# Kernel tuning notes

Measured on AMD Instinct MI355X. Metric: run time of the kernel, lower is better.

## Reference

```python
import jax, jax.numpy as jnp
import numpy as np


def _mlp(x, w1, b1, w2, b2):
    # Linear->ReLU->Linear->ReLU (torch Linear: y = x @ W.T + b)
    return jax.nn.relu(jax.nn.relu(x @ w1.T + b1) @ w2.T + b2)


def _lstm_cell(x, h, c, wih, whh, bih, bhh):
    g = x @ wih.T + bih + h @ whh.T + bhh
    i, f, gg, o = jnp.split(g, 4, axis=-1)  # torch gate order i,f,g,o
    c = jax.nn.sigmoid(f) * c + jax.nn.sigmoid(i) * jnp.tanh(gg)
    h = jax.nn.sigmoid(o) * jnp.tanh(c)
    return h, c


def _decode(iml, img_features, mlp1_w1, mlp1_b1, mlp1_w2, mlp1_b2,
            mlp2_w1, mlp2_b1, mlp2_w2, mlp2_b2,
            lstm_wih, lstm_whh, lstm_bih, lstm_bhh,
            attn_w, attn_b, fc_w, fc_b, emb, max_seq_len):
    # iml: [B, H, K] flattened conv map; annotations are channel vectors per position
    ann = jnp.transpose(iml, (0, 2, 1))          # [B, K, H]
    mean_ann = jnp.mean(iml, axis=-1)            # [B, H]
    h0 = _mlp(mean_ann, mlp1_w1, mlp1_b1, mlp1_w2, mlp1_b2)
    c0 = _mlp(mean_ann, mlp2_w1, mlp2_b1, mlp2_w2, mlp2_b2)
    H = h0.shape[-1]
    # attn = Linear(2H, 1) on cat(ann, h): decompose into two dot products.
    w_a, w_h = attn_w[:H], attn_w[H:]
    e_ann = ann @ w_a + attn_b[0]                # [B, K], annotation part precomputed

    def step(carry, _):
        x, h, c = carry
        h, c = _lstm_cell(x, h, c, lstm_wih, lstm_whh, lstm_bih, lstm_bhh)
        e = e_ann + (h @ w_h)[:, None]           # [B, K] fused concat+linear scores
        alpha = jax.nn.softmax(e, axis=-1)       # [B, K]
        cs = jnp.einsum('bk,bkh->bh', alpha, ann)  # weighted context [B, H]
        logits = jnp.concatenate([h, cs], axis=-1) @ fc_w.T + fc_b  # [B, V]
        sample = jnp.argmax(logits, axis=-1)     # greedy token
        return (emb[sample], h, c), (logits, sample)

    _, (logits, samples) = jax.lax.scan(step, (img_features, h0, c0), None, length=max_seq_len)
    # scan stacks on axis 0 (time); move to [B, T, ...]
    return jnp.transpose(logits, (1, 0, 2)), jnp.transpose(samples, (1, 0))


def setup_inputs() -> dict:
    B, K, H, E, V, T = 64, 196, 512, 512, 10000, 30
    key = jax.random.key(0)
    ks = jax.random.split(key, 11)
    inv = 1.0 / np.sqrt(H)
    r = lambda i, shape, scale=1.0: jax.random.normal(ks[i], shape, jnp.float32) * scale
    return {
        'iml': r(0, (B, H, K)),
        'img_features': r(1, (B, E)),
        'mlp1_w1': r(2, (H, H), inv), 'mlp1_b1': jnp.zeros(H, jnp.float32),
        'mlp1_w2': r(3, (H, H), inv), 'mlp1_b2': jnp.zeros(H, jnp.float32),
        'mlp2_w1': r(4, (H, H), inv), 'mlp2_b1': jnp.zeros(H, jnp.float32),
        'mlp2_w2': r(5, (H, H), inv), 'mlp2_b2': jnp.zeros(H, jnp.float32),
        'lstm_wih': r(6, (4 * H, E), inv), 'lstm_whh': r(7, (4 * H, H), inv),
        'lstm_bih': jnp.zeros(4 * H, jnp.float32), 'lstm_bhh': jnp.zeros(4 * H, jnp.float32),
        'attn_w': r(8, (2 * H,), inv), 'attn_b': jnp.zeros(1, jnp.float32),
        'fc_w': r(9, (V, 2 * H), inv), 'fc_b': jnp.zeros(V, jnp.float32),
        'emb': r(10, (V, E)),
        'max_seq_len': T,
    }


def reference(iml, img_features, mlp1_w1, mlp1_b1, mlp1_w2, mlp1_b2,
              mlp2_w1, mlp2_b1, mlp2_w2, mlp2_b2,
              lstm_wih, lstm_whh, lstm_bih, lstm_bhh,
              attn_w, attn_b, fc_w, fc_b, emb, max_seq_len):
    all_logits, sampled_ids = _decode(
        iml, img_features, mlp1_w1, mlp1_b1, mlp1_w2, mlp1_b2,
        mlp2_w1, mlp2_b1, mlp2_w2, mlp2_b2,
        lstm_wih, lstm_whh, lstm_bih, lstm_bhh,
        attn_w, attn_b, fc_w, fc_b, emb, max_seq_len)
    return all_logits, sampled_ids
```

## Files before the change

kernel.cpp:

```cpp
#include <hip/hip_runtime.h>
#include <hip/hip_bf16.h>

#define B 64
#define KDIM 196
#define H 512
#define V 10000
#define TSTEPS 30
#define VP 10240
#define NVC 40
#define NSLOT 8
#define SLOTSTRIDE 16
#define NT 256

typedef unsigned long long u64;
typedef unsigned int u32;

__device__ __forceinline__ u64 pack_vi(float v, int idx) {
    u32 kb = __float_as_uint(v);
    kb = (kb & 0x80000000u) ? ~kb : (kb | 0x80000000u);
    return ((u64)kb << 32) | (u32)(~(u32)idx);
}
__device__ __forceinline__ u32 best_idx_of_slots(const u64* __restrict__ slots, int b) {
    u64 best = slots[b * SLOTSTRIDE];
#pragma unroll
    for (int s = 1; s < NSLOT; ++s) { u64 v = slots[b * SLOTSTRIDE + s]; if (v > best) best = v; }
    return ~(u32)best;
}


__global__ void k_transpose_fc(const float* __restrict__ fcw, float* __restrict__ dst, int coloff) {
    __shared__ float tile[32][33];
    int v0 = blockIdx.x * 32, i0 = blockIdx.y * 32;
    int tx = threadIdx.x, ty = threadIdx.y;
#pragma unroll
    for (int r = 0; r < 32; r += 8) {
        int v = v0 + ty + r; int i = i0 + tx;
        tile[ty + r][tx] = (v < V) ? fcw[(size_t)v * 1024 + coloff + i] : 0.f;
    }
    __syncthreads();
#pragma unroll
    for (int r = 0; r < 32; r += 8) {
        int i = i0 + ty + r; int v = v0 + tx;
        dst[(size_t)i * VP + v] = tile[tx][ty + r];
    }
}

__global__ void k_build_wct(const float* __restrict__ wih, const float* __restrict__ whh,
                            float* __restrict__ dst) {
    __shared__ float tile[32][33];
    int j0 = blockIdx.x * 32, i0 = blockIdx.y * 32;
    int tx = threadIdx.x, ty = threadIdx.y;
#pragma unroll
    for (int r = 0; r < 32; r += 8) {
        int j = j0 + ty + r; int i = i0 + tx;
        tile[ty + r][tx] = (i < 512) ? wih[(size_t)j * 512 + i] : whh[(size_t)j * 512 + i - 512];
    }
    __syncthreads();
#pragma unroll
    for (int r = 0; r < 32; r += 8) {
        int i = i0 + ty + r; int j = j0 + tx;
        dst[(size_t)i * 2048 + j] = tile[tx][ty + r];
    }
}

__global__ void k_e_alpha(const float* __restrict__ iml, const float* __restrict__ attn_w,
                          float* __restrict__ alpha) {
    int b = blockIdx.x, t = threadIdx.x;
    __shared__ float wa[512];
    wa[t] = attn_w[t]; wa[t + 256] = attn_w[t + 256];
    __syncthreads();
    float acc = 0.f;
    if (t < KDIM) {
        const float* p = iml + (size_t)b * 512 * KDIM + t;
#pragma unroll 8
        for (int h = 0; h < 512; ++h) acc += p[(size_t)h * KDIM] * wa[h];
    }
    __shared__ float red[256];
    red[t] = (t < KDIM) ? acc : -__builtin_inff();
    __syncthreads();
    for (int s = 128; s; s >>= 1) { if (t < s) red[t] = fmaxf(red[t], red[t + s]); __syncthreads(); }
    float mx = red[0];
    __syncthreads();
    float ex = (t < KDIM) ? expf(acc - mx) : 0.f;
    red[t] = ex; __syncthreads();
    for (int s = 128; s; s >>= 1) { if (t < s) red[t] += red[t + s]; __syncthreads(); }
    if (t < KDIM) alpha[b * KDIM + t] = ex / red[0];
}

__global__ void k_mean_cs(const float* __restrict__ iml, const float* __restrict__ alpha,
                          float* __restrict__ mean, float* __restrict__ cs) {
    int w = threadIdx.x >> 6, lane = threadIdx.x & 63;
    int row = blockIdx.x * 4 + w;
    int b = row >> 9;
    const float* p = iml + (size_t)row * KDIM;
    const float* al = alpha + b * KDIM;
    float p0 = p[lane], p1 = p[lane + 64], p2 = p[lane + 128];
    float p3 = (lane < 4) ? p[lane + 192] : 0.f;
    float a3 = (lane < 4) ? al[lane + 192] : 0.f;
    float sm = p0 + p1 + p2 + p3;
    float sc = p0 * al[lane] + p1 * al[lane + 64] + p2 * al[lane + 128] + p3 * a3;
#pragma unroll
    for (int off = 32; off; off >>= 1) { sm += __shfl_down(sm, off); sc += __shfl_down(sc, off); }
    if (lane == 0) { mean[row] = sm * (1.f / 196.f); cs[row] = sc; }
}

__global__ void k_dense_relu2(const float* __restrict__ in0, const float* __restrict__ in1,
                              const float* __restrict__ W0, const float* __restrict__ W1,
                              const float* __restrict__ bi0, const float* __restrict__ bi1,
                              float* __restrict__ o0, float* __restrict__ o1) {
    int z = blockIdx.z;
    const float* in = z ? in1 : in0;
    const float* W  = z ? W1 : W0;
    const float* bias = z ? bi1 : bi0;
    float* out = z ? o1 : o0;
    int b = blockIdx.y; int j = blockIdx.x * 256 + threadIdx.x;
    __shared__ float xs[512];
    xs[threadIdx.x] = in[b * 512 + threadIdx.x];
    xs[threadIdx.x + 256] = in[b * 512 + threadIdx.x + 256];
    __syncthreads();
    float acc = bias[j];
    const float4* w4 = (const float4*)(W + (size_t)j * 512);
#pragma unroll 4
    for (int i4 = 0; i4 < 128; ++i4) {
        float4 w = w4[i4];
        float4 x = *(const float4*)&xs[i4 * 4];
        acc += w.x * x.x + w.y * x.y + w.z * x.z + w.w * x.w;
    }
    out[(size_t)b * 512 + j] = fmaxf(acc, 0.f);
}

__global__ void k_gemm_big(const float* __restrict__ A, int astride,
                           const float* __restrict__ Wt, int wn,
                           float* __restrict__ part) {
    int jb = blockIdx.x, kc = blockIdx.y, bh = blockIdx.z;
    int w = threadIdx.x >> 6, lane = threadIdx.x & 63;
    int b0 = __builtin_amdgcn_readfirstlane(bh * 32 + w * 8);
    int k0 = kc * 64;
    int j0 = jb * 256 + lane * 4;
    float4 acc[8];
#pragma unroll
    for (int b = 0; b < 8; ++b) acc[b] = make_float4(0.f, 0.f, 0.f, 0.f);
    const float* wp = Wt + (size_t)k0 * wn + j0;
    const float* xp = A + (size_t)b0 * astride + k0;
#pragma unroll 8
    for (int kk = 0; kk < 64; ++kk) {
        float4 w4 = *(const float4*)(wp + (size_t)kk * wn);
#pragma unroll
        for (int b = 0; b < 8; ++b) {
            float xv = xp[(size_t)b * astride + kk];
            acc[b].x += xv * w4.x; acc[b].y += xv * w4.y;
            acc[b].z += xv * w4.z; acc[b].w += xv * w4.w;
        }
    }
#pragma unroll
    for (int b = 0; b < 8; ++b)
        *(float4*)(part + (size_t)(kc * 64 + b0 + b) * wn + j0) = acc[b];
}

__global__ void k_base_finish(const float* __restrict__ lpart, const float* __restrict__ fc_b,
                              float* __restrict__ base, u64* __restrict__ slots) {
    int b = blockIdx.y; int v = blockIdx.x * 256 + threadIdx.x;
    if (v < V) {
        float s = fc_b[v];
#pragma unroll
        for (int c = 0; c < 8; ++c) s += lpart[(size_t)(c * 64 + b) * VP + v];
        base[(size_t)b * VP + v] = s;
    }
    if (blockIdx.x == 0 && blockIdx.y == 0) {
#pragma unroll
        for (int i = 0; i < 4; ++i) slots[threadIdx.x + i * 256] = 0ull;
    }
}


__global__ __launch_bounds__(NT) void k_lstm(
        const float* __restrict__ img, const float* __restrict__ emb,
        const u64* __restrict__ slots, const float* __restrict__ hbuf,
        const float* __restrict__ WcT, float* __restrict__ gpart, int t0) {
    __shared__ float lds[4 * 1024];
    const int jb = blockIdx.x, kc = blockIdx.y, bh = blockIdx.z;
    const int tid = threadIdx.x;
    const int w = __builtin_amdgcn_readfirstlane(tid >> 6), lane = tid & 63;
    const int b0 = bh * 8;
    const int kg0 = kc * 256 + w * 64;
    const float* xp[8];
    if (kg0 < 512) {
        if (t0) {
#pragma unroll
            for (int b = 0; b < 8; ++b) xp[b] = img + (size_t)(b0 + b) * 512 + kg0;
        } else {
#pragma unroll
            for (int b = 0; b < 8; ++b) {
                u32 idx = best_idx_of_slots(slots, b0 + b);
                xp[b] = emb + (size_t)idx * 512 + kg0;
            }
        }
    } else {
#pragma unroll
        for (int b = 0; b < 8; ++b) xp[b] = hbuf + (size_t)(b0 + b) * 512 + (kg0 - 512);
    }
    float2 acc[8];
#pragma unroll
    for (int b = 0; b < 8; ++b) acc[b] = make_float2(0.f, 0.f);
    const float* wp = WcT + (size_t)kg0 * 2048 + jb * 128 + lane * 2;
#pragma unroll 8
    for (int kk = 0; kk < 64; ++kk) {
        float2 wv = *(const float2*)(wp + (size_t)kk * 2048);
#pragma unroll
        for (int b = 0; b < 8; ++b) {
            float xv = xp[b][kk];
            acc[b].x += xv * wv.x; acc[b].y += xv * wv.y;
        }
    }
#pragma unroll
    for (int b = 0; b < 8; ++b)
        *(float2*)&lds[w * 1024 + b * 128 + lane * 2] = acc[b];
    __syncthreads();
    {
        const int bl = tid >> 5;
        const int jj = (tid & 31) * 4;
        float4 s = make_float4(0.f, 0.f, 0.f, 0.f);
#pragma unroll
        for (int wv = 0; wv < 4; ++wv) {
            float4 p = *(const float4*)&lds[wv * 1024 + bl * 128 + jj];
            s.x += p.x; s.y += p.y; s.z += p.z; s.w += p.w;
        }
        *(float4*)&gpart[(size_t)(kc * 64 + b0 + bl) * 2048 + jb * 128 + jj] = s;
    }
}

__global__ void k_gates(const float* __restrict__ gpart, const float* __restrict__ bih,
                        const float* __restrict__ bhh, float* __restrict__ hbuf,
                        float* __restrict__ cbuf, u64* __restrict__ slots,
                        float* __restrict__ out1, int t) {
    int e = blockIdx.x * 256 + threadIdx.x;
    int b = e >> 9, jj = e & 511;
    float g[4];
#pragma unroll
    for (int gg = 0; gg < 4; ++gg) {
        int j = jj + gg * 512;
        float s = bih[j] + bhh[j];
#pragma unroll
        for (int kc = 0; kc < 4; ++kc) s += gpart[(size_t)(kc * 64 + b) * 2048 + j];
        g[gg] = s;
    }
    float ig = 1.f / (1.f + expf(-g[0]));
    float fg = 1.f / (1.f + expf(-g[1]));
    float gt = tanhf(g[2]);
    float og = 1.f / (1.f + expf(-g[3]));
    float c = fg * cbuf[e] + ig * gt;
    float h = og * tanhf(c);
    cbuf[e] = c; hbuf[e] = h;
    if (blockIdx.x == 0) {
        if (t > 0 && threadIdx.x < 64)
            out1[threadIdx.x * TSTEPS + (t - 1)] = (float)best_idx_of_slots(slots, threadIdx.x);
        __syncthreads();
        for (int i = threadIdx.x; i < B * SLOTSTRIDE; i += 256) slots[i] = 0ull;
    }
}

__global__ __launch_bounds__(NT) void k_logits_fullk(
        const float* __restrict__ hbuf, const float* __restrict__ fcT,
        const float* __restrict__ base, float* __restrict__ out0,
        u64* __restrict__ slots, int t) {
    __shared__ float lds[4 * 1280];
    const int jb = blockIdx.x, bh = blockIdx.y;
    const int tid = threadIdx.x;
    const int w = __builtin_amdgcn_readfirstlane(tid >> 6), lane = tid & 63;
    const int b0 = bh * 8;
    const int kg0 = w * 128;
    float2 a2[8]; float a1[8];
#pragma unroll
    for (int b = 0; b < 8; ++b) { a2[b] = make_float2(0.f, 0.f); a1[b] = 0.f; }
    const float* wp2 = fcT + (size_t)kg0 * VP + jb * 160 + lane * 2;
    const float* wp1 = fcT + (size_t)kg0 * VP + jb * 160 + 128 + (lane & 31);
    const float* hb0 = hbuf + (size_t)b0 * 512 + kg0;
#pragma unroll 4
    for (int kk = 0; kk < 128; ++kk) {
        float2 w2 = *(const float2*)(wp2 + (size_t)kk * VP);
        float w1 = wp1[(size_t)kk * VP];
#pragma unroll
        for (int b = 0; b < 8; ++b) {
            float xv = hb0[b * 512 + kk];
            a2[b].x += xv * w2.x; a2[b].y += xv * w2.y; a1[b] += xv * w1;
        }
    }
#pragma unroll
    for (int b = 0; b < 8; ++b)
        *(float2*)&lds[w * 1280 + b * 160 + lane * 2] = a2[b];
    if (lane < 32) {
#pragma unroll
        for (int b = 0; b < 8; ++b) lds[w * 1280 + b * 160 + 128 + lane] = a1[b];
    }
    __syncthreads();
    {
        const int bl = tid >> 5;
        const int jj0 = (tid & 31) * 5;
        const int bg = b0 + bl;
        const int j0 = jb * 160 + jj0;
        float m = -__builtin_inff(); int mi = 0x7fffffff;
        if (j0 < V) {
            float* op = out0 + ((size_t)bg * TSTEPS + t) * V + j0;
            const float* bp = base + (size_t)bg * VP + j0;
#pragma unroll
            for (int i = 0; i < 5; ++i) {
                float s = 0.f;
#pragma unroll
                for (int wv = 0; wv < 4; ++wv) s += lds[wv * 1280 + bl * 160 + jj0 + i];
                float val = s + bp[i];
                op[i] = val;
                if (val > m) { m = val; mi = j0 + i; }
            }
        }
#pragma unroll
        for (int mk = 1; mk < 32; mk <<= 1) {
            float ov = __shfl_xor(m, mk);
            int oi = __shfl_xor(mi, mk);
            if (ov > m || (ov == m && oi < mi)) { m = ov; mi = oi; }
        }
        if ((lane & 31) == 0)
            atomicMax(&slots[bg * SLOTSTRIDE + (jb & 7)], pack_vi(m, mi));
    }
}

__global__ void k_final_out1(const u64* __restrict__ slots, float* __restrict__ out1) {
    int b = threadIdx.x;
    if (b < B) out1[b * TSTEPS + (TSTEPS - 1)] = (float)best_idx_of_slots(slots, b);
}


extern "C" void kernel_launch(void* const* d_in, const int* in_sizes, int n_in,
                              void* d_out, int out_size, void* d_ws, size_t ws_size,
                              hipStream_t stream) {
    const float* iml   = (const float*)d_in[0];
    const float* img   = (const float*)d_in[1];
    const float* m1w1  = (const float*)d_in[2];
    const float* m1b1  = (const float*)d_in[3];
    const float* m1w2  = (const float*)d_in[4];
    const float* m1b2  = (const float*)d_in[5];
    const float* m2w1  = (const float*)d_in[6];
    const float* m2b1  = (const float*)d_in[7];
    const float* m2w2  = (const float*)d_in[8];
    const float* m2b2  = (const float*)d_in[9];
    const float* wih   = (const float*)d_in[10];
    const float* whh   = (const float*)d_in[11];
    const float* bih   = (const float*)d_in[12];
    const float* bhh   = (const float*)d_in[13];
    const float* attnw = (const float*)d_in[14];
    const float* fcw   = (const float*)d_in[16];
    const float* fcb   = (const float*)d_in[17];
    const float* emb   = (const float*)d_in[18];

    float* out0 = (float*)d_out;
    float* out1 = out0 + (size_t)B * TSTEPS * V;

    float* ws = (float*)d_ws;
    size_t off = 0;
    float* fcT   = ws + off; off += (size_t)512 * VP;
    float* WcT   = ws + off; off += (size_t)1024 * 2048;
    float* bigp  = ws + off; off += (size_t)8 * B * VP;
    float* gpart = ws + off; off += (size_t)4 * B * 2048;
    float* base  = ws + off; off += (size_t)B * VP;
    float* meanb = ws + off; off += B * 512;
    float* alpha = ws + off; off += B * KDIM;
    float* csb   = ws + off; off += B * 512;
    float* tmp1  = ws + off; off += B * 512;
    float* tmp2  = ws + off; off += B * 512;
    float* hbuf  = ws + off; off += B * 512;
    float* cbuf  = ws + off; off += B * 512;
    u64*   slots = (u64*)(ws + off); off += B * SLOTSTRIDE * 2;

    k_e_alpha<<<dim3(64), dim3(256), 0, stream>>>(iml, attnw, alpha);
    k_mean_cs<<<dim3(8192), dim3(256), 0, stream>>>(iml, alpha, meanb, csb);
    k_dense_relu2<<<dim3(2, 64, 2), dim3(256), 0, stream>>>(meanb, meanb, m1w1, m2w1, m1b1, m2b1, tmp1, tmp2);
    k_dense_relu2<<<dim3(2, 64, 2), dim3(256), 0, stream>>>(tmp1, tmp2, m1w2, m2w2, m1b2, m2b2, hbuf, cbuf);
    k_transpose_fc<<<dim3(VP / 32, 16), dim3(32, 8), 0, stream>>>(fcw, fcT, 512);
    k_gemm_big<<<dim3(40, 8, 2), dim3(256), 0, stream>>>(csb, 512, fcT, VP, bigp);
    k_base_finish<<<dim3(NVC, 64), dim3(256), 0, stream>>>(bigp, fcb, base, slots);
    k_transpose_fc<<<dim3(VP / 32, 16), dim3(32, 8), 0, stream>>>(fcw, fcT, 0);
    k_build_wct<<<dim3(64, 32), dim3(32, 8), 0, stream>>>(wih, whh, WcT);

    for (int t = 0; t < TSTEPS; ++t) {
        k_lstm<<<dim3(16, 4, 8), dim3(NT), 0, stream>>>(img, emb, slots, hbuf, WcT, gpart, (t == 0) ? 1 : 0);
        k_gates<<<dim3(128), dim3(256), 0, stream>>>(gpart, bih, bhh, hbuf, cbuf, slots, out1, t);
        k_logits_fullk<<<dim3(64, 8), dim3(NT), 0, stream>>>(hbuf, fcT, base, out0, slots, t);
    }
    k_final_out1<<<dim3(1), dim3(64), 0, stream>>>(slots, out1);
}
```

Measured before the change: 1.342 ms.

## Fuse LSTM gate activation into logits kernel with double-buffered state

Removes the separate per-step gates kernel. Each logits block now rebuilds the h vectors for its 8 batch rows from the gate partial sums and keeps them in shared memory. The cell state and the argmax slots are double-buffered, so the redundant per-block gate work causes no races, and the slot reset and output write move into the LSTM kernel. The attention score reduction is also split across more blocks, and the bias sum is precomputed. The cost is that every one of the 64 column blocks recomputes the gates, which repeats gpart reads and transcendental math, traded against one fewer launch and sync per step.

```diff
diff --git a/kernel.cpp b/kernel.cpp
--- a/kernel.cpp
+++ b/kernel.cpp
@@ -10,6 +10,7 @@
 #define NVC 40
 #define NSLOT 8
 #define SLOTSTRIDE 16
+#define SLOTBUF (B * SLOTSTRIDE)
 #define NT 256
 
 typedef unsigned long long u64;
@@ -63,17 +64,33 @@
     }
 }
 
-__global__ void k_e_alpha(const float* __restrict__ iml, const float* __restrict__ attn_w,
-                          float* __restrict__ alpha) {
+__global__ void k_bsum(const float* __restrict__ bih, const float* __restrict__ bhh,
+                       float* __restrict__ bsum) {
+    int j = blockIdx.x * 256 + threadIdx.x;
+    bsum[j] = bih[j] + bhh[j];
+}
+
+__global__ void k_e_part(const float* __restrict__ iml, const float* __restrict__ attn_w,
+                         float* __restrict__ epart) {
+    int b = blockIdx.x, hc = blockIdx.y, t = threadIdx.x;
+    __shared__ float wa[64];
+    if (t < 64) wa[t] = attn_w[hc * 64 + t];
+    __syncthreads();
+    if (t < KDIM) {
+        const float* p = iml + (size_t)b * 512 * KDIM + (size_t)hc * 64 * KDIM + t;
+        float acc = 0.f;
+#pragma unroll 8
+        for (int h = 0; h < 64; ++h) acc += p[(size_t)h * KDIM] * wa[h];
+        epart[(size_t)(b * 8 + hc) * 208 + t] = acc;
+    }
+}
+
+__global__ void k_e_softmax(const float* __restrict__ epart, float* __restrict__ alpha) {
     int b = blockIdx.x, t = threadIdx.x;
-    __shared__ float wa[512];
-    wa[t] = attn_w[t]; wa[t + 256] = attn_w[t + 256];
-    __syncthreads();
     float acc = 0.f;
     if (t < KDIM) {
-        const float* p = iml + (size_t)b * 512 * KDIM + t;
-#pragma unroll 8
-        for (int h = 0; h < 512; ++h) acc += p[(size_t)h * KDIM] * wa[h];
+#pragma unroll
+        for (int c = 0; c < 8; ++c) acc += epart[(size_t)(b * 8 + c) * 208 + t];
     }
     __shared__ float red[256];
     red[t] = (t < KDIM) ? acc : -__builtin_inff();
@@ -175,8 +192,9 @@
 
 __global__ __launch_bounds__(NT) void k_lstm(
         const float* __restrict__ img, const float* __restrict__ emb,
-        const u64* __restrict__ slots, const float* __restrict__ hbuf,
-        const float* __restrict__ WcT, float* __restrict__ gpart, int t0) {
+        const u64* __restrict__ slotsR, u64* __restrict__ slotsW,
+        const float* __restrict__ hbuf, const float* __restrict__ WcT,
+        float* __restrict__ gpart, float* __restrict__ out1, int t) {
     __shared__ float lds[4 * 1024];
     const int jb = blockIdx.x, kc = blockIdx.y, bh = blockIdx.z;
     const int tid = threadIdx.x;
@@ -185,13 +203,13 @@
     const int kg0 = kc * 256 + w * 64;
     const float* xp[8];
     if (kg0 < 512) {
-        if (t0) {
+        if (t == 0) {
 #pragma unroll
             for (int b = 0; b < 8; ++b) xp[b] = img + (size_t)(b0 + b) * 512 + kg0;
         } else {
 #pragma unroll
             for (int b = 0; b < 8; ++b) {
-                u32 idx = best_idx_of_slots(slots, b0 + b);
+                u32 idx = best_idx_of_slots(slotsR, b0 + b);
                 xp[b] = emb + (size_t)idx * 512 + kg0;
             }
         }
@@ -227,61 +245,65 @@
         }
         *(float4*)&gpart[(size_t)(kc * 64 + b0 + bl) * 2048 + jb * 128 + jj] = s;
     }
-}
-
-__global__ void k_gates(const float* __restrict__ gpart, const float* __restrict__ bih,
-                        const float* __restrict__ bhh, float* __restrict__ hbuf,
-                        float* __restrict__ cbuf, u64* __restrict__ slots,
-                        float* __restrict__ out1, int t) {
-    int e = blockIdx.x * 256 + threadIdx.x;
-    int b = e >> 9, jj = e & 511;
-    float g[4];
-#pragma unroll
-    for (int gg = 0; gg < 4; ++gg) {
-        int j = jj + gg * 512;
-        float s = bih[j] + bhh[j];
-#pragma unroll
-        for (int kc = 0; kc < 4; ++kc) s += gpart[(size_t)(kc * 64 + b) * 2048 + j];
-        g[gg] = s;
-    }
-    float ig = 1.f / (1.f + expf(-g[0]));
-    float fg = 1.f / (1.f + expf(-g[1]));
-    float gt = tanhf(g[2]);
-    float og = 1.f / (1.f + expf(-g[3]));
-    float c = fg * cbuf[e] + ig * gt;
-    float h = og * tanhf(c);
-    cbuf[e] = c; hbuf[e] = h;
-    if (blockIdx.x == 0) {
-        if (t > 0 && threadIdx.x < 64)
-            out1[threadIdx.x * TSTEPS + (t - 1)] = (float)best_idx_of_slots(slots, threadIdx.x);
-        __syncthreads();
-        for (int i = threadIdx.x; i < B * SLOTSTRIDE; i += 256) slots[i] = 0ull;
-    }
-}
-
-__global__ __launch_bounds__(NT) void k_logits_fullk(
-        const float* __restrict__ hbuf, const float* __restrict__ fcT,
+    if (jb == 0 && kc == 0 && t > 0 && tid < 8)
+        out1[(b0 + tid) * TSTEPS + (t - 1)] = (float)best_idx_of_slots(slotsR, b0 + tid);
+    if (jb == 1 && kc == 0 && bh == 0) {
+#pragma unroll
+        for (int i = 0; i < 4; ++i) slotsW[tid + i * 256] = 0ull;
+    }
+}
+
+__global__ __launch_bounds__(NT) void k_fused(
+        const float* __restrict__ gpart, const float* __restrict__ bsum,
+        const float* __restrict__ cbufR, float* __restrict__ cbufW,
+        float* __restrict__ hbuf, const float* __restrict__ fcT,
         const float* __restrict__ base, float* __restrict__ out0,
-        u64* __restrict__ slots, int t) {
+        u64* __restrict__ slotsW, int t) {
+    __shared__ float hs[8 * 512];
     __shared__ float lds[4 * 1280];
     const int jb = blockIdx.x, bh = blockIdx.y;
     const int tid = threadIdx.x;
+    const int b0 = bh * 8;
+#pragma unroll 4
+    for (int e = tid; e < 4096; e += NT) {
+        int b = e >> 9, jj = e & 511;
+        float g[4];
+#pragma unroll
+        for (int gg = 0; gg < 4; ++gg) {
+            int j = jj + gg * 512;
+            float s = bsum[j];
+#pragma unroll
+            for (int kc = 0; kc < 4; ++kc) s += gpart[(size_t)(kc * 64 + b0 + b) * 2048 + j];
+            g[gg] = s;
+        }
+        float ig = 1.f / (1.f + expf(-g[0]));
+        float fg = 1.f / (1.f + expf(-g[1]));
+        float gt = tanhf(g[2]);
+        float og = 1.f / (1.f + expf(-g[3]));
+        float c = fg * cbufR[(size_t)(b0 + b) * 512 + jj] + ig * gt;
+        float h = og * tanhf(c);
+        hs[b * 512 + jj] = h;
+        if (jb == 0) {
+            cbufW[(size_t)(b0 + b) * 512 + jj] = c;
+            hbuf[(size_t)(b0 + b) * 512 + jj] = h;
+        }
+    }
+    __syncthreads();
     const int w = __builtin_amdgcn_readfirstlane(tid >> 6), lane = tid & 63;
-    const int b0 = bh * 8;
     const int kg0 = w * 128;
     float2 a2[8]; float a1[8];
 #pragma unroll
     for (int b = 0; b < 8; ++b) { a2[b] = make_float2(0.f, 0.f); a1[b] = 0.f; }
     const float* wp2 = fcT + (size_t)kg0 * VP + jb * 160 + lane * 2;
     const float* wp1 = fcT + (size_t)kg0 * VP + jb * 160 + 128 + (lane & 31);
-    const float* hb0 = hbuf + (size_t)b0 * 512 + kg0;
+    const float* hsw = &hs[kg0];
 #pragma unroll 4
     for (int kk = 0; kk < 128; ++kk) {
         float2 w2 = *(const float2*)(wp2 + (size_t)kk * VP);
         float w1 = wp1[(size_t)kk * VP];
 #pragma unroll
         for (int b = 0; b < 8; ++b) {
-            float xv = hb0[b * 512 + kk];
+            float xv = hsw[b * 512 + kk];
             a2[b].x += xv * w2.x; a2[b].y += xv * w2.y; a1[b] += xv * w1;
         }
     }
@@ -318,8 +340,8 @@
             int oi = __shfl_xor(mi, mk);
             if (ov > m || (ov == m && oi < mi)) { m = ov; mi = oi; }
         }
-        if ((lane & 31) == 0)
-            atomicMax(&slots[bg * SLOTSTRIDE + (jb & 7)], pack_vi(m, mi));
+        if ((tid & 31) == 0)
+            atomicMax(&slotsW[bg * SLOTSTRIDE + (jb & 7)], pack_vi(m, mi));
     }
 }
 
@@ -361,16 +383,19 @@
     float* bigp  = ws + off; off += (size_t)8 * B * VP;
     float* gpart = ws + off; off += (size_t)4 * B * 2048;
     float* base  = ws + off; off += (size_t)B * VP;
+    float* epart = ws + off; off += (size_t)B * 8 * 208;
+    float* bsum  = ws + off; off += 2048;
     float* meanb = ws + off; off += B * 512;
     float* alpha = ws + off; off += B * KDIM;
     float* csb   = ws + off; off += B * 512;
     float* tmp1  = ws + off; off += B * 512;
     float* tmp2  = ws + off; off += B * 512;
     float* hbuf  = ws + off; off += B * 512;
-    float* cbuf  = ws + off; off += B * 512;
-    u64*   slots = (u64*)(ws + off); off += B * SLOTSTRIDE * 2;
-
-    k_e_alpha<<<dim3(64), dim3(256), 0, stream>>>(iml, attnw, alpha);
+    float* cbuf  = ws + off; off += (size_t)2 * B * 512;
+    u64*   slots = (u64*)(ws + off); off += 2 * SLOTBUF * 2;
+
+    k_e_part<<<dim3(64, 8), dim3(256), 0, stream>>>(iml, attnw, epart);
+    k_e_softmax<<<dim3(64), dim3(256), 0, stream>>>(epart, alpha);
     k_mean_cs<<<dim3(8192), dim3(256), 0, stream>>>(iml, alpha, meanb, csb);
     k_dense_relu2<<<dim3(2, 64, 2), dim3(256), 0, stream>>>(meanb, meanb, m1w1, m2w1, m1b1, m2b1, tmp1, tmp2);
     k_dense_relu2<<<dim3(2, 64, 2), dim3(256), 0, stream>>>(tmp1, tmp2, m1w2, m2w2, m1b2, m2b2, hbuf, cbuf);
@@ -379,11 +404,16 @@
     k_base_finish<<<dim3(NVC, 64), dim3(256), 0, stream>>>(bigp, fcb, base, slots);
     k_transpose_fc<<<dim3(VP / 32, 16), dim3(32, 8), 0, stream>>>(fcw, fcT, 0);
     k_build_wct<<<dim3(64, 32), dim3(32, 8), 0, stream>>>(wih, whh, WcT);
+    k_bsum<<<dim3(8), dim3(256), 0, stream>>>(bih, bhh, bsum);
 
     for (int t = 0; t < TSTEPS; ++t) {
-        k_lstm<<<dim3(16, 4, 8), dim3(NT), 0, stream>>>(img, emb, slots, hbuf, WcT, gpart, (t == 0) ? 1 : 0);
-        k_gates<<<dim3(128), dim3(256), 0, stream>>>(gpart, bih, bhh, hbuf, cbuf, slots, out1, t);
-        k_logits_fullk<<<dim3(64, 8), dim3(NT), 0, stream>>>(hbuf, fcT, base, out0, slots, t);
-    }
-    k_final_out1<<<dim3(1), dim3(64), 0, stream>>>(slots, out1);
-}
+        int p = t & 1;
+        u64* slotsR = slots + (p ^ 1) * SLOTBUF;
+        u64* slotsW = slots + p * SLOTBUF;
+        float* cbufR = cbuf + p * (B * 512);
+        float* cbufW = cbuf + (p ^ 1) * (B * 512);
+        k_lstm<<<dim3(16, 4, 8), dim3(NT), 0, stream>>>(img, emb, slotsR, slotsW, hbuf, WcT, gpart, out1, t);
+        k_fused<<<dim3(64, 8), dim3(NT), 0, stream>>>(gpart, bsum, cbufR, cbufW, hbuf, fcT, base, out0, slotsW, t);
+    }
+    k_final_out1<<<dim3(1), dim3(64), 0, stream>>>(slots + ((TSTEPS - 1) & 1) * SLOTBUF, out1);
+}
```

After: 1.612 ms. +20.1%, slower.

## Retile per-step logits GEMM to 32x32 blocks and split attention score kernel

Applied to the files above, without the earlier changes.

The per-step logits kernel moves from 160-column by 8-batch tiles to 32-column by 32-batch tiles. Each thread now computes a 4x4 register block using float4 weight loads, so every weight element fetched is reused across more batch rows. Epilogue stores and the argmax reduction are vectorized, and the grid changes from 64x8 to 320x2 blocks. Separately, the one-time attention score computation is split over 8 H-chunks and a small softmax kernel, giving the first pass more parallelism at the cost of one extra launch and a workspace buffer.

```diff
diff --git a/kernel.cpp b/kernel.cpp
--- a/kernel.cpp
+++ b/kernel.cpp
@@ -63,17 +63,27 @@
     }
 }
 
-__global__ void k_e_alpha(const float* __restrict__ iml, const float* __restrict__ attn_w,
-                          float* __restrict__ alpha) {
+__global__ void k_e_part(const float* __restrict__ iml, const float* __restrict__ attn_w,
+                         float* __restrict__ epart) {
+    int b = blockIdx.x, hc = blockIdx.y, t = threadIdx.x;
+    __shared__ float wa[64];
+    if (t < 64) wa[t] = attn_w[hc * 64 + t];
+    __syncthreads();
+    if (t < KDIM) {
+        const float* p = iml + (size_t)b * 512 * KDIM + (size_t)hc * 64 * KDIM + t;
+        float acc = 0.f;
+#pragma unroll 8
+        for (int h = 0; h < 64; ++h) acc += p[(size_t)h * KDIM] * wa[h];
+        epart[(size_t)(b * 8 + hc) * 208 + t] = acc;
+    }
+}
+
+__global__ void k_e_softmax(const float* __restrict__ epart, float* __restrict__ alpha) {
     int b = blockIdx.x, t = threadIdx.x;
-    __shared__ float wa[512];
-    wa[t] = attn_w[t]; wa[t + 256] = attn_w[t + 256];
-    __syncthreads();
     float acc = 0.f;
     if (t < KDIM) {
-        const float* p = iml + (size_t)b * 512 * KDIM + t;
-#pragma unroll 8
-        for (int h = 0; h < 512; ++h) acc += p[(size_t)h * KDIM] * wa[h];
+#pragma unroll
+        for (int c = 0; c < 8; ++c) acc += epart[(size_t)(b * 8 + c) * 208 + t];
     }
     __shared__ float red[256];
     red[t] = (t < KDIM) ? acc : -__builtin_inff();
@@ -259,67 +269,64 @@
     }
 }
 
-__global__ __launch_bounds__(NT) void k_logits_fullk(
+__global__ __launch_bounds__(NT) void k_logits2(
         const float* __restrict__ hbuf, const float* __restrict__ fcT,
         const float* __restrict__ base, float* __restrict__ out0,
         u64* __restrict__ slots, int t) {
-    __shared__ float lds[4 * 1280];
+    __shared__ float lds[4 * 32 * 32];
     const int jb = blockIdx.x, bh = blockIdx.y;
     const int tid = threadIdx.x;
     const int w = __builtin_amdgcn_readfirstlane(tid >> 6), lane = tid & 63;
-    const int b0 = bh * 8;
+    const int j0 = jb * 32, b0 = bh * 32;
+    const int jg = lane & 7, bg = lane >> 3;
     const int kg0 = w * 128;
-    float2 a2[8]; float a1[8];
-#pragma unroll
-    for (int b = 0; b < 8; ++b) { a2[b] = make_float2(0.f, 0.f); a1[b] = 0.f; }
-    const float* wp2 = fcT + (size_t)kg0 * VP + jb * 160 + lane * 2;
-    const float* wp1 = fcT + (size_t)kg0 * VP + jb * 160 + 128 + (lane & 31);
-    const float* hb0 = hbuf + (size_t)b0 * 512 + kg0;
-#pragma unroll 4
+    float4 acc[4];
+#pragma unroll
+    for (int i = 0; i < 4; ++i) acc[i] = make_float4(0.f, 0.f, 0.f, 0.f);
+    const float* wp = fcT + (size_t)kg0 * VP + j0 + jg * 4;
+    const float* hp = hbuf + (size_t)(b0 + bg * 4) * 512 + kg0;
+#pragma unroll 8
     for (int kk = 0; kk < 128; ++kk) {
-        float2 w2 = *(const float2*)(wp2 + (size_t)kk * VP);
-        float w1 = wp1[(size_t)kk * VP];
-#pragma unroll
-        for (int b = 0; b < 8; ++b) {
-            float xv = hb0[b * 512 + kk];
-            a2[b].x += xv * w2.x; a2[b].y += xv * w2.y; a1[b] += xv * w1;
-        }
-    }
-#pragma unroll
-    for (int b = 0; b < 8; ++b)
-        *(float2*)&lds[w * 1280 + b * 160 + lane * 2] = a2[b];
-    if (lane < 32) {
-#pragma unroll
-        for (int b = 0; b < 8; ++b) lds[w * 1280 + b * 160 + 128 + lane] = a1[b];
-    }
+        float4 w4 = *(const float4*)(wp + (size_t)kk * VP);
+        float h0 = hp[kk], h1 = hp[512 + kk], h2 = hp[1024 + kk], h3 = hp[1536 + kk];
+        acc[0].x += h0 * w4.x; acc[0].y += h0 * w4.y; acc[0].z += h0 * w4.z; acc[0].w += h0 * w4.w;
+        acc[1].x += h1 * w4.x; acc[1].y += h1 * w4.y; acc[1].z += h1 * w4.z; acc[1].w += h1 * w4.w;
+        acc[2].x += h2 * w4.x; acc[2].y += h2 * w4.y; acc[2].z += h2 * w4.z; acc[2].w += h2 * w4.w;
+        acc[3].x += h3 * w4.x; acc[3].y += h3 * w4.y; acc[3].z += h3 * w4.z; acc[3].w += h3 * w4.w;
+    }
+#pragma unroll
+    for (int i = 0; i < 4; ++i)
+        *(float4*)&lds[(w * 32 + bg * 4 + i) * 32 + jg * 4] = acc[i];
     __syncthreads();
     {
-        const int bl = tid >> 5;
-        const int jj0 = (tid & 31) * 5;
-        const int bg = b0 + bl;
-        const int j0 = jb * 160 + jj0;
+        const int bl = tid >> 3;
+        const int jg2 = tid & 7;
+        const int bgl = b0 + bl;
+        const int j = j0 + jg2 * 4;
+        float4 s = make_float4(0.f, 0.f, 0.f, 0.f);
+#pragma unroll
+        for (int wv = 0; wv < 4; ++wv) {
+            float4 p = *(const float4*)&lds[(wv * 32 + bl) * 32 + jg2 * 4];
+            s.x += p.x; s.y += p.y; s.z += p.z; s.w += p.w;
+        }
         float m = -__builtin_inff(); int mi = 0x7fffffff;
-        if (j0 < V) {
-            float* op = out0 + ((size_t)bg * TSTEPS + t) * V + j0;
-            const float* bp = base + (size_t)bg * VP + j0;
-#pragma unroll
-            for (int i = 0; i < 5; ++i) {
-                float s = 0.f;
-#pragma unroll
-                for (int wv = 0; wv < 4; ++wv) s += lds[wv * 1280 + bl * 160 + jj0 + i];
-                float val = s + bp[i];
-                op[i] = val;
-                if (val > m) { m = val; mi = j0 + i; }
-            }
-        }
-#pragma unroll
-        for (int mk = 1; mk < 32; mk <<= 1) {
+        if (j < V) {
+            float4 bs = *(const float4*)(base + (size_t)bgl * VP + j);
+            float4 val = make_float4(s.x + bs.x, s.y + bs.y, s.z + bs.z, s.w + bs.w);
+            *(float4*)(out0 + ((size_t)bgl * TSTEPS + t) * V + j) = val;
+            m = val.x; mi = j;
+            if (val.y > m) { m = val.y; mi = j + 1; }
+            if (val.z > m) { m = val.z; mi = j + 2; }
+            if (val.w > m) { m = val.w; mi = j + 3; }
+        }
+#pragma unroll
+        for (int mk = 1; mk < 8; mk <<= 1) {
             float ov = __shfl_xor(m, mk);
             int oi = __shfl_xor(mi, mk);
             if (ov > m || (ov == m && oi < mi)) { m = ov; mi = oi; }
         }
-        if ((lane & 31) == 0)
-            atomicMax(&slots[bg * SLOTSTRIDE + (jb & 7)], pack_vi(m, mi));
+        if (jg2 == 0)
+            atomicMax(&slots[bgl * SLOTSTRIDE + (jb & 7)], pack_vi(m, mi));
     }
 }
 
@@ -361,6 +368,7 @@
     float* bigp  = ws + off; off += (size_t)8 * B * VP;
     float* gpart = ws + off; off += (size_t)4 * B * 2048;
     float* base  = ws + off; off += (size_t)B * VP;
+    float* epart = ws + off; off += (size_t)B * 8 * 208;
     float* meanb = ws + off; off += B * 512;
     float* alpha = ws + off; off += B * KDIM;
     float* csb   = ws + off; off += B * 512;
@@ -370,7 +378,8 @@
     float* cbuf  = ws + off; off += B * 512;
     u64*   slots = (u64*)(ws + off); off += B * SLOTSTRIDE * 2;
 
-    k_e_alpha<<<dim3(64), dim3(256), 0, stream>>>(iml, attnw, alpha);
+    k_e_part<<<dim3(64, 8), dim3(256), 0, stream>>>(iml, attnw, epart);
+    k_e_softmax<<<dim3(64), dim3(256), 0, stream>>>(epart, alpha);
     k_mean_cs<<<dim3(8192), dim3(256), 0, stream>>>(iml, alpha, meanb, csb);
     k_dense_relu2<<<dim3(2, 64, 2), dim3(256), 0, stream>>>(meanb, meanb, m1w1, m2w1, m1b1, m2b1, tmp1, tmp2);
     k_dense_relu2<<<dim3(2, 64, 2), dim3(256), 0, stream>>>(tmp1, tmp2, m1w2, m2w2, m1b2, m2b2, hbuf, cbuf);
@@ -383,7 +392,7 @@
     for (int t = 0; t < TSTEPS; ++t) {
         k_lstm<<<dim3(16, 4, 8), dim3(NT), 0, stream>>>(img, emb, slots, hbuf, WcT, gpart, (t == 0) ? 1 : 0);
         k_gates<<<dim3(128), dim3(256), 0, stream>>>(gpart, bih, bhh, hbuf, cbuf, slots, out1, t);
-        k_logits_fullk<<<dim3(64, 8), dim3(NT), 0, stream>>>(hbuf, fcT, base, out0, slots, t);
+        k_logits2<<<dim3(320, 2), dim3(NT), 0, stream>>>(hbuf, fcT, base, out0, slots, t);
     }
     k_final_out1<<<dim3(1), dim3(64), 0, stream>>>(slots, out1);
 }
```

After: 1.616 ms. 1.2x slower.
